# Performance work log

Measured on AMD Instinct MI355X. Metric: run time of the kernel, lower is better.

The kernel has to match this reference:

```python
import jax, jax.numpy as jnp
import numpy as np

B, N, D, H, K = 8, 1024, 1024, 64, 20


def setup_inputs() -> dict:
    key = jax.random.key(0)
    ks = jax.random.split(key, 8)
    s = 0.05
    return {
        "f1": jax.random.normal(ks[0], (B, N, D), jnp.float32),
        "f2": jax.random.normal(ks[1], (B, N, D), jnp.float32),
        "W1a": jax.random.normal(ks[2], (D, H), jnp.float32) * s,
        "b1a": jnp.zeros((H,), jnp.float32),
        "W2a": jax.random.normal(ks[3], (H, H), jnp.float32) * s,
        "b2a": jnp.zeros((H,), jnp.float32),
        "W1b": jax.random.normal(ks[4], (H, H), jnp.float32) * s,
        "b1b": jnp.zeros((H,), jnp.float32),
        "W2b": jax.random.normal(ks[5], (H, H), jnp.float32) * s,
        "b2b": jnp.zeros((H,), jnp.float32),
        "k": K,
    }


def _knn_idx(f, k):
    # f: [N, D] -> indices [N, k] of k nearest neighbors (self excluded)
    sq = jnp.sum(f * f, axis=-1)                      # [N]
    d = sq[:, None] + sq[None, :] - 2.0 * (f @ f.T)   # [N, N] squared dists
    n = f.shape[0]
    d = d + jnp.eye(n, dtype=f.dtype) * jnp.float32(1e10)  # exclude self-loop
    _, idx = jax.lax.top_k(-d, k)                     # smallest distances
    return idx


def _gin_layer(x, idx, W1, b1, W2, b2):
    # GINConv with eps=0: MLP(x + sum_{j in N(i)} x_j)
    agg = jnp.sum(x[idx], axis=1)                     # [N, D] neighbor-sum
    h = x + agg
    h = jnp.maximum(h @ W1 + b1, 0.0) @ W2 + b2
    return h


def reference(f1, f2, W1a, b1a, W2a, b2a, W1b, b1b, W2b, b2b, k):
    def encode(f):
        idx = _knn_idx(f, k)
        h = _gin_layer(f, idx, W1a, b1a, W2a, b2a)
        h = _gin_layer(h, idx, W1b, b1b, W2b, b2b)
        return h

    def per_sample(a, b):
        z1 = encode(a)                                # [N, H]
        z2 = encode(b)                                # [N, H]
        sim = z1 @ z2.T                               # [N, N]
        return jax.nn.softmax(sim, axis=1)

    return jax.vmap(per_sample)(f1, f2)               # [B, N, N]
```

## Files before the change

### kernel.cpp

```cpp
#include <hip/hip_runtime.h>
#include <hip/hip_bf16.h>
#include <math.h>

#define BATCH 8
#define NPTS  1024
#define DIM   1024
#define HID   64
#define KNN   20
#define NMAT  16
#define KPACK 3072

typedef __attribute__((ext_vector_type(8))) short short8;
typedef __attribute__((ext_vector_type(4))) float floatx4;

__device__ __forceinline__ const float* mat_base(const float* f1, const float* f2, int m) {
    return (m < BATCH) ? (f1 + (size_t)m * NPTS * DIM)
                       : (f2 + (size_t)(m - BATCH) * NPTS * DIM);
}

__device__ __forceinline__ unsigned short f2bf_bits(float v) {
    __hip_bfloat16 h = __float2bfloat16(v);
    return *(unsigned short*)&h;
}
__device__ __forceinline__ float bfbits2f(unsigned short b) {
    union { unsigned u; float f; } c; c.u = ((unsigned)b) << 16; return c.f;
}

__global__ __launch_bounds__(256) void split_kernel(const float* __restrict__ f1,
                                                    const float* __restrict__ f2,
                                                    unsigned short* __restrict__ H,
                                                    float* __restrict__ sq) {
    int tid = threadIdx.x;
    int wave = tid >> 6, lane = tid & 63;
    int row = blockIdx.x * 4 + wave;
    int m = row >> 10, i = row & (NPTS - 1);
    const float* fr = mat_base(f1, f2, m) + (size_t)i * DIM;
    unsigned short* Hr = H + (size_t)row * KPACK;
    float s = 0.f;
    #pragma unroll
    for (int t = 0; t < 4; ++t) {
        int idx = t * 256 + lane * 4;
        float4 v = *(const float4*)&fr[idx];
        s += v.x * v.x + v.y * v.y + v.z * v.z + v.w * v.w;
        unsigned short h1[4], h2[4], h3[4];
        float vv[4] = {v.x, v.y, v.z, v.w};
        #pragma unroll
        for (int c = 0; c < 4; ++c) {
            unsigned short b1 = f2bf_bits(vv[c]);
            float r1 = vv[c] - bfbits2f(b1);
            unsigned short b2 = f2bf_bits(r1);
            float r2 = r1 - bfbits2f(b2);
            unsigned short b3 = f2bf_bits(r2);
            h1[c] = b1; h2[c] = b2; h3[c] = b3;
        }
        *(ushort4*)&Hr[idx]        = *(ushort4*)&h1[0];
        *(ushort4*)&Hr[1024 + idx] = *(ushort4*)&h2[0];
        *(ushort4*)&Hr[2048 + idx] = *(ushort4*)&h3[0];
    }
    #pragma unroll
    for (int o = 32; o > 0; o >>= 1) s += __shfl_down(s, o);
    if (lane == 0) sq[row] = s;
}

__global__ __launch_bounds__(256) void gram_mfma_kernel(const unsigned short* __restrict__ H,
                                                        const float* __restrict__ sq,
                                                        float* __restrict__ dist) {
    int bid = blockIdx.x;
    int xcd = bid & 7;
    int g = bid >> 3;
    int m = xcd + 8 * (g & 1);
    int t = g >> 1;
    int bi = 0;
    { int a = t; while (a >= 8 - bi) { a -= 8 - bi; ++bi; } t = a; }
    int bj = bi + t;
    int ti = bi << 7, tj = bj << 7;

    const unsigned short* Hm = H + (size_t)m * NPTS * KPACK;

    __shared__ __align__(16) unsigned short Asl[24 * 512];
    __shared__ __align__(16) unsigned short Bsl[24 * 512];

    int tid = threadIdx.x;
    int w = tid >> 6, lane = tid & 63;
    int wi = w >> 1, wj = w & 1;
    int r16 = lane & 15, kc = lane >> 4;

    floatx4 acc[4][4];
    #pragma unroll
    for (int a = 0; a < 4; ++a)
        #pragma unroll
        for (int b = 0; b < 4; ++b) acc[a][b] = (floatx4)0.f;

    for (int kk = 0; kk < 1024; kk += 32) {
        __syncthreads();
        #pragma unroll
        for (int c = 0; c < 6; ++c) {
            int ca = w * 6 + c;
            int seg = ca >> 3;
            int rb  = ca & 7;
            size_t koff = (size_t)(seg << 10) + kk + kc * 8;
            const unsigned short* ga = Hm + (size_t)(ti + rb * 16 + r16) * KPACK + koff;
            const unsigned short* gb = Hm + (size_t)(tj + rb * 16 + r16) * KPACK + koff;
            __builtin_amdgcn_global_load_lds(
                (const __attribute__((address_space(1))) void*)ga,
                (__attribute__((address_space(3))) void*)&Asl[ca * 512], 16, 0, 0);
            __builtin_amdgcn_global_load_lds(
                (const __attribute__((address_space(1))) void*)gb,
                (__attribute__((address_space(3))) void*)&Bsl[ca * 512], 16, 0, 0);
        }
        __syncthreads();
        short8 af[3][4];
        #pragma unroll
        for (int s = 0; s < 3; ++s)
            #pragma unroll
            for (int a = 0; a < 4; ++a)
                af[s][a] = *(const short8*)&Asl[(s * 8 + wi * 4 + a) * 512 + lane * 8];
        #pragma unroll
        for (int sb = 0; sb < 3; ++sb) {
            short8 bf[4];
            #pragma unroll
            for (int b = 0; b < 4; ++b)
                bf[b] = *(const short8*)&Bsl[(sb * 8 + wj * 4 + b) * 512 + lane * 8];
            #pragma unroll
            for (int sa = 0; sa < 3; ++sa) {
                if (sa + sb > 2) continue;
                #pragma unroll
                for (int a = 0; a < 4; ++a)
                    #pragma unroll
                    for (int b = 0; b < 4; ++b)
                        acc[a][b] = __builtin_amdgcn_mfma_f32_16x16x32_bf16(af[sa][a], bf[b], acc[a][b], 0, 0, 0);
            }
        }
    }

    const float* sqm = sq + m * NPTS;
    #pragma unroll
    for (int a = 0; a < 4; ++a) {
        int i0 = ti + wi * 64 + a * 16 + (lane >> 4) * 4;
        #pragma unroll
        for (int b = 0; b < 4; ++b) {
            int j = tj + wj * 64 + b * 16 + (lane & 15);
            float sqj = sqm[j];
            #pragma unroll
            for (int r = 0; r < 4; ++r) {
                int i = i0 + r;
                float v = sqm[i] + sqj - 2.f * acc[a][b][r];
                if (i == j) v += 1e10f;
                dist[((size_t)m * NPTS + i) * NPTS + j] = v;
                if (bi != bj) dist[((size_t)m * NPTS + j) * NPTS + i] = v;
            }
        }
    }
}

__global__ __launch_bounds__(256) void topk_kernel(const float* __restrict__ dist,
                                                   int* __restrict__ knn_idx) {
    int tid = threadIdx.x;
    int wave = tid >> 6, lane = tid & 63;
    int row = blockIdx.x * 4 + wave;
    const float* d = dist + (size_t)row * NPTS;
    float v[16];
    #pragma unroll
    for (int s = 0; s < 16; ++s) v[s] = d[s * 64 + lane];
    int myj = 0;
    for (int sel = 0; sel < KNN; ++sel) {
        float bv = v[0]; int bs = 0;
        #pragma unroll
        for (int s = 1; s < 16; ++s)
            if (v[s] < bv) { bv = v[s]; bs = s; }
        int bj = bs * 64 + lane;
        #pragma unroll
        for (int off = 1; off < 64; off <<= 1) {
            float ov = __shfl_xor(bv, off);
            int   oj = __shfl_xor(bj, off);
            if (ov < bv || (ov == bv && oj < bj)) { bv = ov; bj = oj; }
        }
        if ((bj & 63) == lane) v[bj >> 6] = 3e38f;
        if (lane == sel) myj = bj;
    }
    if (lane < KNN) knn_idx[(size_t)row * KNN + lane] = myj;
}

__global__ __launch_bounds__(256) void ymlp_kernel(const float* __restrict__ f1,
                                                   const float* __restrict__ f2,
                                                   const float* __restrict__ W,
                                                   float* __restrict__ y) {
    int row0 = blockIdx.x * 64;
    int m = row0 >> 10;
    const float* A = mat_base(f1, f2, m) + (size_t)(row0 & (NPTS - 1)) * DIM;
    __shared__ float As[64][20];
    __shared__ float Ws[16][HID];
    int tid = threadIdx.x;
    int ty = tid >> 4, tx = tid & 15;
    float acc[4][4];
    #pragma unroll
    for (int i = 0; i < 4; ++i)
        #pragma unroll
        for (int j = 0; j < 4; ++j) acc[i][j] = 0.f;
    for (int kk = 0; kk < DIM; kk += 16) {
        {
            int r = tid >> 2, c = (tid & 3) * 4;
            *(float4*)&As[r][c] = *(const float4*)&A[(size_t)r * DIM + kk + c];
        }
        {
            int d = tid >> 4, hh = (tid & 15) * 4;
            *(float4*)&Ws[d][hh] = *(const float4*)&W[(size_t)(kk + d) * HID + hh];
        }
        __syncthreads();
        #pragma unroll
        for (int k = 0; k < 16; ++k) {
            float a[4];
            #pragma unroll
            for (int ii = 0; ii < 4; ++ii) a[ii] = As[ty * 4 + ii][k];
            float4 w = *(const float4*)&Ws[k][tx * 4];
            #pragma unroll
            for (int ii = 0; ii < 4; ++ii) {
                acc[ii][0] += a[ii] * w.x;
                acc[ii][1] += a[ii] * w.y;
                acc[ii][2] += a[ii] * w.z;
                acc[ii][3] += a[ii] * w.w;
            }
        }
        __syncthreads();
    }
    #pragma unroll
    for (int ii = 0; ii < 4; ++ii)
        *(float4*)&y[(size_t)(row0 + ty * 4 + ii) * HID + tx * 4] = *(float4*)&acc[ii][0];
}

__global__ __launch_bounds__(256) void t1h1_kernel(const float* __restrict__ y,
                                                   const int* __restrict__ knn_idx,
                                                   const float* __restrict__ W,
                                                   const float* __restrict__ bias1,
                                                   const float* __restrict__ bias2,
                                                   float* __restrict__ h1) {
    int row0 = blockIdx.x * 64;
    int m = row0 >> 10;
    __shared__ int nb[64 * KNN];
    __shared__ float t1s[64][65];
    __shared__ float Ws[64][HID];
    __shared__ float b1s[HID], b2s[HID];
    int tid = threadIdx.x;
    for (int k = tid; k < 64 * KNN; k += 256) nb[k] = knn_idx[(size_t)row0 * KNN + k];
    for (int k = tid; k < 64 * HID; k += 256) Ws[k >> 6][k & 63] = W[k];
    if (tid < HID) { b1s[tid] = bias1[tid]; b2s[tid] = bias2[tid]; }
    __syncthreads();
    {
        int r = tid >> 2, c0 = (tid & 3) * 16;
        const float* yr = y + (size_t)(row0 + r) * HID + c0;
        float4 a[4];
        #pragma unroll
        for (int q = 0; q < 4; ++q) a[q] = *(const float4*)&yr[q * 4];
        const float* ym = y + (size_t)(m << 10) * HID;
        #pragma unroll
        for (int t = 0; t < KNN; ++t) {
            const float* yn = ym + (size_t)nb[r * KNN + t] * HID + c0;
            #pragma unroll
            for (int q = 0; q < 4; ++q) {
                float4 v = *(const float4*)&yn[q * 4];
                a[q].x += v.x; a[q].y += v.y; a[q].z += v.z; a[q].w += v.w;
            }
        }
        #pragma unroll
        for (int q = 0; q < 4; ++q) {
            int c = c0 + q * 4;
            t1s[r][c + 0] = fmaxf(a[q].x + b1s[c + 0], 0.f);
            t1s[r][c + 1] = fmaxf(a[q].y + b1s[c + 1], 0.f);
            t1s[r][c + 2] = fmaxf(a[q].z + b1s[c + 2], 0.f);
            t1s[r][c + 3] = fmaxf(a[q].w + b1s[c + 3], 0.f);
        }
    }
    __syncthreads();
    int ty = tid >> 4, tx = tid & 15;
    float acc[4][4];
    #pragma unroll
    for (int i = 0; i < 4; ++i)
        #pragma unroll
        for (int j = 0; j < 4; ++j) acc[i][j] = 0.f;
    #pragma unroll
    for (int k = 0; k < HID; ++k) {
        float a[4];
        #pragma unroll
        for (int ii = 0; ii < 4; ++ii) a[ii] = t1s[ty * 4 + ii][k];
        float4 w = *(const float4*)&Ws[k][tx * 4];
        #pragma unroll
        for (int ii = 0; ii < 4; ++ii) {
            acc[ii][0] += a[ii] * w.x;
            acc[ii][1] += a[ii] * w.y;
            acc[ii][2] += a[ii] * w.z;
            acc[ii][3] += a[ii] * w.w;
        }
    }
    #pragma unroll
    for (int ii = 0; ii < 4; ++ii) {
        float o[4];
        #pragma unroll
        for (int jj = 0; jj < 4; ++jj) o[jj] = acc[ii][jj] + b2s[tx * 4 + jj];
        *(float4*)&h1[(size_t)(row0 + ty * 4 + ii) * HID + tx * 4] = *(float4*)&o[0];
    }
}

__global__ __launch_bounds__(256) void t2z_kernel(const float* __restrict__ h1,
                                                  const int* __restrict__ knn_idx,
                                                  const float* __restrict__ W1,
                                                  const float* __restrict__ bias1,
                                                  const float* __restrict__ W2,
                                                  const float* __restrict__ bias2,
                                                  float* __restrict__ z) {
    int row0 = blockIdx.x * 64;
    int m = row0 >> 10;
    __shared__ int nb[64 * KNN];
    __shared__ float hs[64][65];
    __shared__ float t2s[64][65];
    __shared__ float Ws[64][HID];
    __shared__ float b1s[HID], b2s[HID];
    int tid = threadIdx.x;
    for (int k = tid; k < 64 * KNN; k += 256) nb[k] = knn_idx[(size_t)row0 * KNN + k];
    for (int k = tid; k < 64 * HID; k += 256) Ws[k >> 6][k & 63] = W1[k];
    if (tid < HID) { b1s[tid] = bias1[tid]; b2s[tid] = bias2[tid]; }
    __syncthreads();
    {
        int r = tid >> 2, c0 = (tid & 3) * 16;
        const float* hr = h1 + (size_t)(row0 + r) * HID + c0;
        float4 a[4];
        #pragma unroll
        for (int q = 0; q < 4; ++q) a[q] = *(const float4*)&hr[q * 4];
        const float* hm = h1 + (size_t)(m << 10) * HID;
        #pragma unroll
        for (int t = 0; t < KNN; ++t) {
            const float* hn = hm + (size_t)nb[r * KNN + t] * HID + c0;
            #pragma unroll
            for (int q = 0; q < 4; ++q) {
                float4 v = *(const float4*)&hn[q * 4];
                a[q].x += v.x; a[q].y += v.y; a[q].z += v.z; a[q].w += v.w;
            }
        }
        #pragma unroll
        for (int q = 0; q < 4; ++q) *(float4*)&hs[r][c0 + q * 4] = a[q];
    }
    __syncthreads();
    int ty = tid >> 4, tx = tid & 15;
    float acc[4][4];
    #pragma unroll
    for (int i = 0; i < 4; ++i)
        #pragma unroll
        for (int j = 0; j < 4; ++j) acc[i][j] = 0.f;
    #pragma unroll
    for (int k = 0; k < HID; ++k) {
        float a[4];
        #pragma unroll
        for (int ii = 0; ii < 4; ++ii) a[ii] = hs[ty * 4 + ii][k];
        float4 w = *(const float4*)&Ws[k][tx * 4];
        #pragma unroll
        for (int ii = 0; ii < 4; ++ii) {
            acc[ii][0] += a[ii] * w.x;
            acc[ii][1] += a[ii] * w.y;
            acc[ii][2] += a[ii] * w.z;
            acc[ii][3] += a[ii] * w.w;
        }
    }
    #pragma unroll
    for (int ii = 0; ii < 4; ++ii)
        #pragma unroll
        for (int jj = 0; jj < 4; ++jj)
            t2s[ty * 4 + ii][tx * 4 + jj] = fmaxf(acc[ii][jj] + b1s[tx * 4 + jj], 0.f);
    __syncthreads();
    for (int k = tid; k < 64 * HID; k += 256) Ws[k >> 6][k & 63] = W2[k];
    __syncthreads();
    #pragma unroll
    for (int i = 0; i < 4; ++i)
        #pragma unroll
        for (int j = 0; j < 4; ++j) acc[i][j] = 0.f;
    #pragma unroll
    for (int k = 0; k < HID; ++k) {
        float a[4];
        #pragma unroll
        for (int ii = 0; ii < 4; ++ii) a[ii] = t2s[ty * 4 + ii][k];
        float4 w = *(const float4*)&Ws[k][tx * 4];
        #pragma unroll
        for (int ii = 0; ii < 4; ++ii) {
            acc[ii][0] += a[ii] * w.x;
            acc[ii][1] += a[ii] * w.y;
            acc[ii][2] += a[ii] * w.z;
            acc[ii][3] += a[ii] * w.w;
        }
    }
    #pragma unroll
    for (int ii = 0; ii < 4; ++ii) {
        float o[4];
        #pragma unroll
        for (int jj = 0; jj < 4; ++jj) o[jj] = acc[ii][jj] + b2s[tx * 4 + jj];
        *(float4*)&z[(size_t)(row0 + ty * 4 + ii) * HID + tx * 4] = *(float4*)&o[0];
    }
}

__global__ __launch_bounds__(256) void sim_kernel(const float* __restrict__ z,
                                                  float* __restrict__ logits) {
    int bid = blockIdx.x;
    int b = bid >> 8;
    int tile = bid & 255;
    int ti = (tile >> 4) << 6;
    int tj = (tile & 15) << 6;
    const float* z1 = z + (size_t)b * NPTS * HID;
    const float* z2 = z + (size_t)(BATCH + b) * NPTS * HID;
    __shared__ float Z1[64][68];
    __shared__ float Z2[64][68];
    int tid = threadIdx.x;
    #pragma unroll
    for (int i = 0; i < 4; ++i) {
        int l = tid + i * 256;
        int r = l >> 4, c = (l & 15) * 4;
        *(float4*)&Z1[r][c] = *(const float4*)&z1[(size_t)(ti + r) * HID + c];
        *(float4*)&Z2[r][c] = *(const float4*)&z2[(size_t)(tj + r) * HID + c];
    }
    __syncthreads();
    int ty = tid >> 4, tx = tid & 15;
    float acc[4][4];
    #pragma unroll
    for (int i = 0; i < 4; ++i)
        #pragma unroll
        for (int j = 0; j < 4; ++j) acc[i][j] = 0.f;
    #pragma unroll
    for (int h = 0; h < HID; ++h) {
        float a[4], bb[4];
        #pragma unroll
        for (int ii = 0; ii < 4; ++ii) { a[ii] = Z1[ty * 4 + ii][h]; bb[ii] = Z2[tx * 4 + ii][h]; }
        #pragma unroll
        for (int ii = 0; ii < 4; ++ii)
            #pragma unroll
            for (int jj = 0; jj < 4; ++jj)
                acc[ii][jj] += a[ii] * bb[jj];
    }
    #pragma unroll
    for (int ii = 0; ii < 4; ++ii) {
        float* dst = logits + ((size_t)b * NPTS + ti + ty * 4 + ii) * NPTS + tj + tx * 4;
        *(float4*)&dst[0] = *(float4*)&acc[ii][0];
    }
}

__global__ __launch_bounds__(256) void softmax_kernel(const float* __restrict__ logits,
                                                      float* __restrict__ out) {
    int row = blockIdx.x;
    const float* L = logits + (size_t)row * NPTS;
    __shared__ float buf[NPTS];
    __shared__ float red[8];
    int tid = threadIdx.x;
    int wave = tid >> 6, lane = tid & 63;
    float mx = -3e38f;
    #pragma unroll
    for (int s = 0; s < 4; ++s) {
        float v = L[tid + s * 256];
        buf[tid + s * 256] = v;
        mx = fmaxf(mx, v);
    }
    #pragma unroll
    for (int off = 32; off > 0; off >>= 1) mx = fmaxf(mx, __shfl_down(mx, off));
    if (lane == 0) red[wave] = mx;
    __syncthreads();
    mx = fmaxf(fmaxf(red[0], red[1]), fmaxf(red[2], red[3]));
    float sum = 0.f;
    #pragma unroll
    for (int s = 0; s < 4; ++s) {
        float e = expf(buf[tid + s * 256] - mx);
        buf[tid + s * 256] = e;
        sum += e;
    }
    #pragma unroll
    for (int off = 32; off > 0; off >>= 1) sum += __shfl_down(sum, off);
    if (lane == 0) red[4 + wave] = sum;
    __syncthreads();
    float inv = 1.f / (red[4] + red[5] + red[6] + red[7]);
    #pragma unroll
    for (int s = 0; s < 4; ++s)
        out[(size_t)row * NPTS + tid + s * 256] = buf[tid + s * 256] * inv;
}

extern "C" void kernel_launch(void* const* d_in, const int* in_sizes, int n_in,
                              void* d_out, int out_size, void* d_ws, size_t ws_size,
                              hipStream_t stream) {
    const float* f1  = (const float*)d_in[0];
    const float* f2  = (const float*)d_in[1];
    const float* W1a = (const float*)d_in[2];
    const float* b1a = (const float*)d_in[3];
    const float* W2a = (const float*)d_in[4];
    const float* b2a = (const float*)d_in[5];
    const float* W1b = (const float*)d_in[6];
    const float* b1b = (const float*)d_in[7];
    const float* W2b = (const float*)d_in[8];
    const float* b2b = (const float*)d_in[9];
    float* out = (float*)d_out;

    char* ws = (char*)d_ws;
    unsigned short* H = (unsigned short*)ws;
    float* dist = (float*)(ws + (size_t)NMAT * NPTS * KPACK * sizeof(unsigned short));
    float* sq   = dist + (size_t)NMAT * NPTS * NPTS;
    int*   kidx = (int*)(sq + NMAT * NPTS);
    float* ybuf = (float*)(kidx + NMAT * NPTS * KNN);
    float* h1b  = ybuf + (size_t)NMAT * NPTS * HID;
    float* zb   = h1b + (size_t)NMAT * NPTS * HID;

    split_kernel<<<NMAT * NPTS / 4, 256, 0, stream>>>(f1, f2, H, sq);
    gram_mfma_kernel<<<NMAT * 36, 256, 0, stream>>>(H, sq, dist);
    topk_kernel<<<NMAT * NPTS / 4, 256, 0, stream>>>(dist, kidx);
    ymlp_kernel<<<NMAT * NPTS / 64, 256, 0, stream>>>(f1, f2, W1a, ybuf);
    t1h1_kernel<<<NMAT * NPTS / 64, 256, 0, stream>>>(ybuf, kidx, W2a, b1a, b2a, h1b);
    t2z_kernel<<<NMAT * NPTS / 64, 256, 0, stream>>>(h1b, kidx, W1b, b1b, W2b, b2b, zb);
    sim_kernel<<<BATCH * 256, 256, 0, stream>>>(zb, dist);
    softmax_kernel<<<BATCH * NPTS, 256, 0, stream>>>(dist, out);
}
```

Before: 540.9 us.

## Split bf16x3 Gram GEMM into two K-passes with smaller LDS tiles

```diff
diff --git a/kernel.cpp b/kernel.cpp
--- a/kernel.cpp
+++ b/kernel.cpp
@@ -62,9 +62,9 @@
     if (lane == 0) sq[row] = s;
 }
 
-__global__ __launch_bounds__(256) void gram_mfma_kernel(const unsigned short* __restrict__ H,
-                                                        const float* __restrict__ sq,
-                                                        float* __restrict__ dist) {
+__global__ __launch_bounds__(256, 3) void gram_mfma_kernel(const unsigned short* __restrict__ H,
+                                                           const float* __restrict__ sq,
+                                                           float* __restrict__ dist) {
     int bid = blockIdx.x;
     int xcd = bid & 7;
     int g = bid >> 3;
@@ -77,8 +77,8 @@
 
     const unsigned short* Hm = H + (size_t)m * NPTS * KPACK;
 
-    __shared__ __align__(16) unsigned short Asl[24 * 512];
-    __shared__ __align__(16) unsigned short Bsl[24 * 512];
+    __shared__ __align__(16) unsigned short Asl[16 * 512];
+    __shared__ __align__(16) unsigned short Bsl[16 * 512];
 
     int tid = threadIdx.x;
     int w = tid >> 6, lane = tid & 63;
@@ -94,43 +94,76 @@
     for (int kk = 0; kk < 1024; kk += 32) {
         __syncthreads();
         #pragma unroll
-        for (int c = 0; c < 6; ++c) {
-            int ca = w * 6 + c;
-            int seg = ca >> 3;
-            int rb  = ca & 7;
-            size_t koff = (size_t)(seg << 10) + kk + kc * 8;
-            const unsigned short* ga = Hm + (size_t)(ti + rb * 16 + r16) * KPACK + koff;
-            const unsigned short* gb = Hm + (size_t)(tj + rb * 16 + r16) * KPACK + koff;
+        for (int c = 0; c < 8; ++c) {
+            int ca = w * 8 + c;
+            int isB = ca >= 16;
+            int cl = ca & 15;
+            int segl = cl >> 3;
+            int rb  = cl & 7;
+            size_t koff = ((size_t)segl << 10) + kk + kc * 8;
+            int baseRow = (isB ? tj : ti) + rb * 16 + r16;
+            const unsigned short* gp = Hm + (size_t)baseRow * KPACK + koff;
+            unsigned short* lp = (isB ? Bsl : Asl) + cl * 512;
             __builtin_amdgcn_global_load_lds(
-                (const __attribute__((address_space(1))) void*)ga,
-                (__attribute__((address_space(3))) void*)&Asl[ca * 512], 16, 0, 0);
-            __builtin_amdgcn_global_load_lds(
-                (const __attribute__((address_space(1))) void*)gb,
-                (__attribute__((address_space(3))) void*)&Bsl[ca * 512], 16, 0, 0);
+                (const __attribute__((address_space(1))) void*)gp,
+                (__attribute__((address_space(3))) void*)lp, 16, 0, 0);
         }
         __syncthreads();
-        short8 af[3][4];
-        #pragma unroll
-        for (int s = 0; s < 3; ++s)
-            #pragma unroll
-            for (int a = 0; a < 4; ++a)
+        short8 af[2][4], bf[2][4];
+        #pragma unroll
+        for (int s = 0; s < 2; ++s)
+            #pragma unroll
+            for (int a = 0; a < 4; ++a) {
                 af[s][a] = *(const short8*)&Asl[(s * 8 + wi * 4 + a) * 512 + lane * 8];
-        #pragma unroll
-        for (int sb = 0; sb < 3; ++sb) {
-            short8 bf[4];
-            #pragma unroll
-            for (int b = 0; b < 4; ++b)
-                bf[b] = *(const short8*)&Bsl[(sb * 8 + wj * 4 + b) * 512 + lane * 8];
-            #pragma unroll
-            for (int sa = 0; sa < 3; ++sa) {
-                if (sa + sb > 2) continue;
+                bf[s][a] = *(const short8*)&Bsl[(s * 8 + wj * 4 + a) * 512 + lane * 8];
+            }
+        #pragma unroll
+        for (int sb = 0; sb < 2; ++sb)
+            #pragma unroll
+            for (int sa = 0; sa < 2; ++sa)
                 #pragma unroll
                 for (int a = 0; a < 4; ++a)
                     #pragma unroll
                     for (int b = 0; b < 4; ++b)
-                        acc[a][b] = __builtin_amdgcn_mfma_f32_16x16x32_bf16(af[sa][a], bf[b], acc[a][b], 0, 0, 0);
+                        acc[a][b] = __builtin_amdgcn_mfma_f32_16x16x32_bf16(af[sa][a], bf[sb][b], acc[a][b], 0, 0, 0);
+    }
+
+    for (int kk = 0; kk < 1024; kk += 32) {
+        __syncthreads();
+        #pragma unroll
+        for (int c = 0; c < 8; ++c) {
+            int ca = w * 8 + c;
+            int isB = ca >= 16;
+            int cl = ca & 15;
+            int segl = cl >> 3;
+            int rb  = cl & 7;
+            size_t koff = ((size_t)(segl ? 2 : 0) << 10) + kk + kc * 8;
+            int baseRow = (isB ? tj : ti) + rb * 16 + r16;
+            const unsigned short* gp = Hm + (size_t)baseRow * KPACK + koff;
+            unsigned short* lp = (isB ? Bsl : Asl) + cl * 512;
+            __builtin_amdgcn_global_load_lds(
+                (const __attribute__((address_space(1))) void*)gp,
+                (__attribute__((address_space(3))) void*)lp, 16, 0, 0);
+        }
+        __syncthreads();
+        short8 af[2][4], bf[2][4];
+        #pragma unroll
+        for (int s = 0; s < 2; ++s)
+            #pragma unroll
+            for (int a = 0; a < 4; ++a) {
+                af[s][a] = *(const short8*)&Asl[(s * 8 + wi * 4 + a) * 512 + lane * 8];
+                bf[s][a] = *(const short8*)&Bsl[(s * 8 + wj * 4 + a) * 512 + lane * 8];
             }
-        }
+        #pragma unroll
+        for (int a = 0; a < 4; ++a)
+            #pragma unroll
+            for (int b = 0; b < 4; ++b)
+                acc[a][b] = __builtin_amdgcn_mfma_f32_16x16x32_bf16(af[1][a], bf[0][b], acc[a][b], 0, 0, 0);
+        #pragma unroll
+        for (int a = 0; a < 4; ++a)
+            #pragma unroll
+            for (int b = 0; b < 4; ++b)
+                acc[a][b] = __builtin_amdgcn_mfma_f32_16x16x32_bf16(af[0][a], bf[1][b], acc[a][b], 0, 0, 0);
     }
 
     const float* sqm = sq + m * NPTS;
```

New measurement: 573.1 us. 5.9% more time.
